# Optimization experiments

Hardware: AMD Instinct MI355X
Metric: run time of the kernel (lower is better)

## Reference

```python
import jax, jax.numpy as jnp
import numpy as np

B, S, D = 8, 2048, 512


def setup_inputs() -> dict:
    key = jax.random.key(0)
    ks = jax.random.split(key, 8)
    batch = jax.random.normal(ks[0], (B, S, D), dtype=jnp.float32)
    lengths = jax.random.randint(ks[1], (B,), 1, S + 1)  # in [1, S], avoid empty rows
    scale = 1.0 / np.sqrt(D)
    wq = jax.random.normal(ks[2], (D, D), dtype=jnp.float32) * scale
    bq = jnp.zeros((D,), dtype=jnp.float32)
    wk = jax.random.normal(ks[3], (D, D), dtype=jnp.float32) * scale
    bk = jnp.zeros((D,), dtype=jnp.float32)
    wv = jax.random.normal(ks[4], (D, D), dtype=jnp.float32) * scale
    bv = jnp.zeros((D,), dtype=jnp.float32)
    return {"batch": batch, "wq": wq, "bq": bq, "wk": wk, "bk": bk,
            "wv": wv, "bv": bv, "lengths": lengths}


def reference(batch, wq, bq, wk, bk, wv, bv, lengths):
    # Linear projections (torch nn.Linear: x @ W.T + b)
    q = batch @ wq.T + bq  # [B,S,D]
    k = batch @ wk.T + bk
    v = batch @ wv.T + bv
    d = batch.shape[-1]
    scores = jnp.einsum('bqd,bkd->bqk', q, k) / jnp.sqrt(jnp.asarray(d, batch.dtype))
    col = jnp.arange(scores.shape[-1])
    row = jnp.arange(scores.shape[-2])
    causal = col[None, :] <= row[:, None]                  # [S,S], allow col <= row
    pad = col[None, None, :] < lengths[:, None, None]      # [B,1,S], allow col < length
    mask = causal[None, :, :] & pad
    scores = jnp.where(mask, scores, -jnp.inf)
    attn = jax.nn.softmax(scores, axis=-1)
    return jnp.einsum('bqk,bkd->bqd', attn, v)
```

## Files before the change

kernel.cpp:

```cpp
#include <hip/hip_runtime.h>


typedef unsigned short u16;
typedef unsigned int u32;
typedef u16 u16x4 __attribute__((ext_vector_type(4)));
typedef float f32x4 __attribute__((ext_vector_type(4)));
typedef __bf16 bf16x8 __attribute__((ext_vector_type(8)));

#define NBATCH 8
#define NS 2048
#define ND 512
#define NM (NBATCH*NS)

typedef __attribute__((address_space(1))) u32 gu32;
typedef __attribute__((address_space(3))) u32 lu32;
#define GLD16(g, l) __builtin_amdgcn_global_load_lds((gu32*)(g), (lu32*)(l), 16, 0, 0)

__device__ __forceinline__ u16 f2bf(float f) {
  union { float f; u32 u; } v; v.f = f;
  u32 r = v.u + 0x7FFFu + ((v.u >> 16) & 1u);
  return (u16)(r >> 16);
}

__device__ __forceinline__ f32x4 mfma16(bf16x8 a, bf16x8 b, f32x4 c) {
  return __builtin_amdgcn_mfma_f32_16x16x32_bf16(a, b, c, 0, 0, 0);
}

__global__ void cvt_kernel(const float* __restrict__ batch,
                           const float* __restrict__ wq,
                           const float* __restrict__ wk,
                           const float* __restrict__ wv,
                           u16* __restrict__ Xb, u16* __restrict__ Wqb,
                           u16* __restrict__ Wkb, u16* __restrict__ Wvb) {
  const int MD4 = NM * ND / 4;
  const int W4 = ND * ND / 4;
  int total = MD4 + 3 * W4;
  for (int i = blockIdx.x * blockDim.x + threadIdx.x; i < total;
       i += gridDim.x * blockDim.x) {
    const float4* src; u16x4* dst; int off;
    if (i < MD4)             { src = (const float4*)batch; dst = (u16x4*)Xb;  off = i; }
    else if (i < MD4 + W4)   { src = (const float4*)wq;    dst = (u16x4*)Wqb; off = i - MD4; }
    else if (i < MD4 + 2*W4) { src = (const float4*)wk;    dst = (u16x4*)Wkb; off = i - MD4 - W4; }
    else                     { src = (const float4*)wv;    dst = (u16x4*)Wvb; off = i - MD4 - 2*W4; }
    float4 v = src[off];
    u16x4 o; o[0] = f2bf(v.x); o[1] = f2bf(v.y); o[2] = f2bf(v.z); o[3] = f2bf(v.w);
    dst[off] = o;
  }
}

__global__ __launch_bounds__(256) void qkv_gemm(
    const u16* __restrict__ Xb,
    const u16* __restrict__ Wqb, const u16* __restrict__ Wkb, const u16* __restrict__ Wvb,
    const float* __restrict__ bq, const float* __restrict__ bk, const float* __restrict__ bv,
    u16* __restrict__ Qb, u16* __restrict__ Kb, u16* __restrict__ Vt) {
  __shared__ u16 Asm[128 * 64];
  __shared__ u16 Bsm[128 * 64];
  int tid = threadIdx.x;
  int w = tid >> 6, lane = tid & 63, la = lane & 15, hi = lane >> 4;
  int wm = w >> 1, wn = w & 1;
  int m0 = blockIdx.x * 128, n0 = blockIdx.y * 128, z = blockIdx.z;
  const u16* W = (z == 0) ? Wqb : (z == 1) ? Wkb : Wvb;
  f32x4 acc[4][4];
  f32x4 zero = {0.f, 0.f, 0.f, 0.f};
#pragma unroll
  for (int mi = 0; mi < 4; ++mi)
#pragma unroll
    for (int ni = 0; ni < 4; ++ni) acc[mi][ni] = zero;

  for (int kt = 0; kt < 8; ++kt) {
#pragma unroll
    for (int i = 0; i < 4; ++i) {
      int c = w * 4 + i;
      int row = c * 8 + (lane >> 3);
      const char* ga = (const char*)Xb + ((size_t)(m0 + row) * ND + kt * 64) * 2 + (lane & 7) * 16;
      GLD16(ga, (char*)Asm + c * 1024);
      const char* gb = (const char*)W + ((size_t)(n0 + row) * ND + kt * 64) * 2 + (lane & 7) * 16;
      GLD16(gb, (char*)Bsm + c * 1024);
    }
    __syncthreads();
#pragma unroll
    for (int kk = 0; kk < 2; ++kk) {
      bf16x8 a[4], bfr[4];
#pragma unroll
      for (int mi = 0; mi < 4; ++mi)
        a[mi] = *(const bf16x8*)((const char*)Asm + (wm * 64 + mi * 16 + la) * 128 + kk * 64 + hi * 16);
#pragma unroll
      for (int ni = 0; ni < 4; ++ni)
        bfr[ni] = *(const bf16x8*)((const char*)Bsm + (wn * 64 + ni * 16 + la) * 128 + kk * 64 + hi * 16);
#pragma unroll
      for (int mi = 0; mi < 4; ++mi)
#pragma unroll
        for (int ni = 0; ni < 4; ++ni)
          acc[mi][ni] = mfma16(a[mi], bfr[ni], acc[mi][ni]);
    }
    __syncthreads();
  }

  const float* bias = (z == 0) ? bq : (z == 1) ? bk : bv;
  float scl = (z == 0) ? 0.044194173824159216f : 1.0f;
#pragma unroll
  for (int mi = 0; mi < 4; ++mi) {
#pragma unroll
    for (int ni = 0; ni < 4; ++ni) {
      int col = n0 + wn * 64 + ni * 16 + la;
      int rbase = m0 + wm * 64 + mi * 16 + hi * 4;
      float bc = bias[col];
      if (z == 2) {
        int bbx = rbase >> 11, s0 = rbase & 2047;
        u16x4 pk;
#pragma unroll
        for (int j = 0; j < 4; ++j) pk[j] = f2bf(acc[mi][ni][j] + bc);
        *(u16x4*)((char*)Vt + (((size_t)bbx * ND + col) * NS + s0) * 2) = pk;
      } else {
        u16* Ob = (z == 0) ? Qb : Kb;
#pragma unroll
        for (int j = 0; j < 4; ++j)
          Ob[(size_t)(rbase + j) * ND + col] = f2bf((acc[mi][ni][j] + bc) * scl);
      }
    }
  }
}

__global__ __launch_bounds__(256, 1) void attn_kernel(
    const u16* __restrict__ Qb, const u16* __restrict__ Kb, const u16* __restrict__ Vt,
    const int* __restrict__ lens, float* __restrict__ out) {
  __shared__ u16 Ksm[64 * 512];
  __shared__ u16 Vsm[512 * 64];
  __shared__ u16 Psm[4][16 * 72];
  int tid = threadIdx.x;
  int w = tid >> 6, lane = tid & 63, la = lane & 15, hi = lane >> 4;
  int b = blockIdx.y, q0 = blockIdx.x * 64;
  int len = lens[b];
  int r0 = q0 + w * 16;
  int qrow = r0 + la;

  bf16x8 qf[16];
  const char* qbase = (const char*)Qb + (size_t)(b * NS + r0 + la) * ND * 2 + hi * 16;
#pragma unroll
  for (int kc = 0; kc < 16; ++kc) qf[kc] = *(const bf16x8*)(qbase + kc * 64);

  f32x4 o[32];
  f32x4 zero = {0.f, 0.f, 0.f, 0.f};
#pragma unroll
  for (int i = 0; i < 32; ++i) o[i] = zero;
  float mrow = -1e30f, lrow = 0.f;

  int kmaxc = min(q0 + 63, len - 1);
  int ntiles = (kmaxc >> 6) + 1;

  for (int t = 0; t < ntiles; ++t) {
    int k0 = t * 64;
#pragma unroll
    for (int i = 0; i < 16; ++i) {
      int r = w * 16 + i;
      const char* g = (const char*)Kb + (size_t)(b * NS + k0 + r) * ND * 2 + ((lane ^ (r & 7)) * 16);
      GLD16(g, (char*)Ksm + r * 1024);
    }
#pragma unroll
    for (int i = 0; i < 16; ++i) {
      int c = w * 16 + i;
      int d = c * 8 + (lane >> 3);
      const char* g = (const char*)Vt + ((size_t)(b * ND + d) * NS + k0) * 2 + (((lane & 7) ^ (d & 7)) * 16);
      GLD16(g, (char*)Vsm + c * 1024);
    }
    __syncthreads();

    f32x4 s[4];
#pragma unroll
    for (int f = 0; f < 4; ++f) s[f] = zero;
#pragma unroll
    for (int kc = 0; kc < 16; ++kc) {
#pragma unroll
      for (int f = 0; f < 4; ++f) {
        int row = f * 16 + la;
        const char* p = (const char*)Ksm + row * 1024 + ((kc * 64 + hi * 16) ^ ((row & 7) * 16));
        bf16x8 kf = *(const bf16x8*)p;
        s[f] = mfma16(kf, qf[kc], s[f]);
      }
    }

    float tmax = -1e30f;
#pragma unroll
    for (int f = 0; f < 4; ++f) {
#pragma unroll
      for (int j = 0; j < 4; ++j) {
        int kabs = k0 + f * 16 + hi * 4 + j;
        bool ok = (kabs <= qrow) && (kabs < len);
        float vv = ok ? s[f][j] : -1e30f;
        s[f][j] = vv;
        tmax = fmaxf(tmax, vv);
      }
    }
    tmax = fmaxf(tmax, __shfl_xor(tmax, 16));
    tmax = fmaxf(tmax, __shfl_xor(tmax, 32));
    float mnew = fmaxf(mrow, tmax);
    float alpha = __expf(mrow - mnew);
    float psum = 0.f;
#pragma unroll
    for (int f = 0; f < 4; ++f) {
#pragma unroll
      for (int j = 0; j < 4; ++j) {
        float p = __expf(s[f][j] - mnew);
        s[f][j] = p;
        psum += p;
      }
    }
    psum += __shfl_xor(psum, 16);
    psum += __shfl_xor(psum, 32);
    lrow = lrow * alpha + psum;
    mrow = mnew;

#pragma unroll
    for (int f = 0; f < 4; ++f) {
      u16x4 pk;
#pragma unroll
      for (int j = 0; j < 4; ++j) pk[j] = f2bf(s[f][j]);
      *(u16x4*)((char*)&Psm[w][0] + la * 144 + (f * 16 + hi * 4) * 2) = pk;
    }

    float aj[4];
#pragma unroll
    for (int j = 0; j < 4; ++j) aj[j] = __shfl(alpha, hi * 4 + j);
#pragma unroll
    for (int nb = 0; nb < 32; ++nb) {
      o[nb][0] *= aj[0]; o[nb][1] *= aj[1]; o[nb][2] *= aj[2]; o[nb][3] *= aj[3];
    }

#pragma unroll
    for (int ks = 0; ks < 2; ++ks) {
      bf16x8 pf = *(const bf16x8*)((const char*)&Psm[w][0] + la * 144 + ks * 64 + hi * 16);
#pragma unroll
      for (int nb = 0; nb < 32; ++nb) {
        int d = nb * 16 + la;
        const char* vp = (const char*)Vsm + d * 128 + ((ks * 64 + hi * 16) ^ ((d & 7) * 16));
        bf16x8 vf = *(const bf16x8*)vp;
        o[nb] = mfma16(pf, vf, o[nb]);
      }
    }
    __syncthreads();
  }

  float linv[4];
#pragma unroll
  for (int j = 0; j < 4; ++j) linv[j] = 1.0f / __shfl(lrow, hi * 4 + j);
  float* ob = out + (size_t)(b * NS + r0 + hi * 4) * ND + la;
#pragma unroll
  for (int nb = 0; nb < 32; ++nb)
#pragma unroll
    for (int j = 0; j < 4; ++j)
      ob[(size_t)j * ND + nb * 16] = o[nb][j] * linv[j];
}

extern "C" void kernel_launch(void* const* d_in, const int* in_sizes, int n_in,
                              void* d_out, int out_size, void* d_ws, size_t ws_size,
                              hipStream_t stream) {
  const float* batch = (const float*)d_in[0];
  const float* wq = (const float*)d_in[1];
  const float* bq = (const float*)d_in[2];
  const float* wk = (const float*)d_in[3];
  const float* bk = (const float*)d_in[4];
  const float* wv = (const float*)d_in[5];
  const float* bv = (const float*)d_in[6];
  const int* lens = (const int*)d_in[7];

  char* ws = (char*)d_ws;
  u16* Xb  = (u16*)(ws + 0);
  u16* Wqb = (u16*)(ws + 16777216);
  u16* Wkb = (u16*)(ws + 17301504);
  u16* Wvb = (u16*)(ws + 17825792);
  u16* Qb  = (u16*)(ws + 18350080);
  u16* Kb  = (u16*)(ws + 35127296);
  u16* Vt  = (u16*)(ws + 51904512);

  cvt_kernel<<<dim3(2048), dim3(256), 0, stream>>>(batch, wq, wk, wv, Xb, Wqb, Wkb, Wvb);
  qkv_gemm<<<dim3(128, 4, 3), dim3(256), 0, stream>>>(Xb, Wqb, Wkb, Wvb, bq, bk, bv, Qb, Kb, Vt);
  attn_kernel<<<dim3(32, 8), dim3(256), 0, stream>>>(Qb, Kb, Vt, lens, (float*)d_out);
}
```

Baseline: 193.4 us.

## Split long causal KV ranges across two blocks, prefetch tiles, and combine partials

```diff
diff --git a/kernel.cpp b/kernel.cpp
--- a/kernel.cpp
+++ b/kernel.cpp
@@ -123,14 +123,34 @@
 
 __global__ __launch_bounds__(256, 1) void attn_kernel(
     const u16* __restrict__ Qb, const u16* __restrict__ Kb, const u16* __restrict__ Vt,
-    const int* __restrict__ lens, float* __restrict__ out) {
+    const int* __restrict__ lens, float* __restrict__ out,
+    float* __restrict__ pO, float* __restrict__ pM, float* __restrict__ pL) {
   __shared__ u16 Ksm[64 * 512];
   __shared__ u16 Vsm[512 * 64];
-  __shared__ u16 Psm[4][16 * 72];
+  __shared__ u16 Psm[64 * 72];
+  __shared__ float Alds[64];
+  __shared__ float Llds[64];
+
+  int bi = blockIdx.x;
+  int qt = 31 - (bi >> 4);
+  int jj0 = bi & 15;
+  int b = jj0 & 7, c = jj0 >> 3;
+  int len = lens[b];
+  int q0 = qt * 64;
+  int kmax = min(q0 + 63, len - 1);
+  int lastT = kmax >> 6;
+  int t0 = c * 16;
+  int t1 = min(lastT + 1, t0 + 16);
+  bool split = (qt >= 16);
+  int slot = split ? ((b * 16 + (qt - 16)) * 2 + c) : 0;
   int tid = threadIdx.x;
   int w = tid >> 6, lane = tid & 63, la = lane & 15, hi = lane >> 4;
-  int b = blockIdx.y, q0 = blockIdx.x * 64;
-  int len = lens[b];
+
+  if (t0 >= t1) {
+    if (split && tid < 64) { pM[slot * 64 + tid] = -1e30f; pL[slot * 64 + tid] = 0.f; }
+    return;
+  }
+
   int r0 = q0 + w * 16;
   int qrow = r0 + la;
 
@@ -139,31 +159,40 @@
 #pragma unroll
   for (int kc = 0; kc < 16; ++kc) qf[kc] = *(const bf16x8*)(qbase + kc * 64);
 
-  f32x4 o[32];
+  f32x4 o[4][8];
   f32x4 zero = {0.f, 0.f, 0.f, 0.f};
 #pragma unroll
-  for (int i = 0; i < 32; ++i) o[i] = zero;
+  for (int qb = 0; qb < 4; ++qb)
+#pragma unroll
+    for (int nb = 0; nb < 8; ++nb) o[qb][nb] = zero;
   float mrow = -1e30f, lrow = 0.f;
 
-  int kmaxc = min(q0 + 63, len - 1);
-  int ntiles = (kmaxc >> 6) + 1;
-
-  for (int t = 0; t < ntiles; ++t) {
+#define STAGE_K(T) {                                                            \
+  _Pragma("unroll")                                                             \
+  for (int i_ = 0; i_ < 16; ++i_) {                                             \
+    int r_ = w * 16 + i_;                                                       \
+    const char* g_ = (const char*)Kb + (size_t)(b * NS + (T) * 64 + r_) * ND * 2 \
+                     + ((lane ^ (r_ & 7)) * 16);                                \
+    GLD16(g_, (char*)Ksm + r_ * 1024);                                          \
+  } }
+#define STAGE_V(T) {                                                            \
+  _Pragma("unroll")                                                             \
+  for (int i_ = 0; i_ < 16; ++i_) {                                             \
+    int c_ = w * 16 + i_;                                                       \
+    int d_ = c_ * 8 + (lane >> 3);                                              \
+    const char* g_ = (const char*)Vt + ((size_t)(b * ND + d_) * NS + (T) * 64) * 2 \
+                     + (((lane & 7) ^ (d_ & 7)) * 16);                          \
+    GLD16(g_, (char*)Vsm + c_ * 1024);                                          \
+  } }
+
+  STAGE_K(t0);
+  STAGE_V(t0);
+
+  for (int t = t0; t < t1; ++t) {
     int k0 = t * 64;
-#pragma unroll
-    for (int i = 0; i < 16; ++i) {
-      int r = w * 16 + i;
-      const char* g = (const char*)Kb + (size_t)(b * NS + k0 + r) * ND * 2 + ((lane ^ (r & 7)) * 16);
-      GLD16(g, (char*)Ksm + r * 1024);
-    }
-#pragma unroll
-    for (int i = 0; i < 16; ++i) {
-      int c = w * 16 + i;
-      int d = c * 8 + (lane >> 3);
-      const char* g = (const char*)Vt + ((size_t)(b * ND + d) * NS + k0) * 2 + (((lane & 7) ^ (d & 7)) * 16);
-      GLD16(g, (char*)Vsm + c * 1024);
-    }
-    __syncthreads();
+    bool more = (t + 1 < t1);
+    asm volatile("s_waitcnt vmcnt(16)" ::: "memory");
+    __builtin_amdgcn_s_barrier();
 
     f32x4 s[4];
 #pragma unroll
@@ -178,6 +207,8 @@
         s[f] = mfma16(kf, qf[kc], s[f]);
       }
     }
+    __builtin_amdgcn_s_barrier();
+    if (more) STAGE_K(t + 1);
 
     float tmax = -1e30f;
 #pragma unroll
@@ -193,7 +224,7 @@
     }
     tmax = fmaxf(tmax, __shfl_xor(tmax, 16));
     tmax = fmaxf(tmax, __shfl_xor(tmax, 32));
-    float mnew = fmaxf(mrow, tmax);
+    float mnew = fmaxf(fmaxf(mrow, tmax), -1e20f);
     float alpha = __expf(mrow - mnew);
     float psum = 0.f;
 #pragma unroll
@@ -215,40 +246,111 @@
       u16x4 pk;
 #pragma unroll
       for (int j = 0; j < 4; ++j) pk[j] = f2bf(s[f][j]);
-      *(u16x4*)((char*)&Psm[w][0] + la * 144 + (f * 16 + hi * 4) * 2) = pk;
-    }
-
-    float aj[4];
-#pragma unroll
-    for (int j = 0; j < 4; ++j) aj[j] = __shfl(alpha, hi * 4 + j);
-#pragma unroll
-    for (int nb = 0; nb < 32; ++nb) {
-      o[nb][0] *= aj[0]; o[nb][1] *= aj[1]; o[nb][2] *= aj[2]; o[nb][3] *= aj[3];
-    }
+      *(u16x4*)((char*)Psm + (w * 16 + la) * 144 + (f * 16 + hi * 4) * 2) = pk;
+    }
+    if (hi == 0) Alds[w * 16 + la] = alpha;
+    asm volatile("s_waitcnt lgkmcnt(0)" ::: "memory");
+    if (more) { asm volatile("s_waitcnt vmcnt(16)" ::: "memory"); }
+    else      { asm volatile("s_waitcnt vmcnt(0)" ::: "memory"); }
+    __builtin_amdgcn_s_barrier();
+
+    float aq[4][4];
+#pragma unroll
+    for (int qb = 0; qb < 4; ++qb)
+#pragma unroll
+      for (int j = 0; j < 4; ++j) aq[qb][j] = Alds[qb * 16 + hi * 4 + j];
+#pragma unroll
+    for (int qb = 0; qb < 4; ++qb)
+#pragma unroll
+      for (int nb = 0; nb < 8; ++nb) {
+        o[qb][nb][0] *= aq[qb][0]; o[qb][nb][1] *= aq[qb][1];
+        o[qb][nb][2] *= aq[qb][2]; o[qb][nb][3] *= aq[qb][3];
+      }
 
 #pragma unroll
     for (int ks = 0; ks < 2; ++ks) {
-      bf16x8 pf = *(const bf16x8*)((const char*)&Psm[w][0] + la * 144 + ks * 64 + hi * 16);
-#pragma unroll
-      for (int nb = 0; nb < 32; ++nb) {
-        int d = nb * 16 + la;
-        const char* vp = (const char*)Vsm + d * 128 + ((ks * 64 + hi * 16) ^ ((d & 7) * 16));
-        bf16x8 vf = *(const bf16x8*)vp;
-        o[nb] = mfma16(pf, vf, o[nb]);
-      }
-    }
-    __syncthreads();
-  }
-
-  float linv[4];
-#pragma unroll
-  for (int j = 0; j < 4; ++j) linv[j] = 1.0f / __shfl(lrow, hi * 4 + j);
-  float* ob = out + (size_t)(b * NS + r0 + hi * 4) * ND + la;
-#pragma unroll
-  for (int nb = 0; nb < 32; ++nb)
-#pragma unroll
-    for (int j = 0; j < 4; ++j)
-      ob[(size_t)j * ND + nb * 16] = o[nb][j] * linv[j];
+      bf16x8 vf[8];
+#pragma unroll
+      for (int nb = 0; nb < 8; ++nb) {
+        int d = w * 128 + nb * 16 + la;
+        vf[nb] = *(const bf16x8*)((const char*)Vsm + d * 128 + ((ks * 64 + hi * 16) ^ ((d & 7) * 16)));
+      }
+#pragma unroll
+      for (int qb = 0; qb < 4; ++qb) {
+        bf16x8 pf = *(const bf16x8*)((const char*)Psm + (qb * 16 + la) * 144 + ks * 64 + hi * 16);
+#pragma unroll
+        for (int nb = 0; nb < 8; ++nb) o[qb][nb] = mfma16(pf, vf[nb], o[qb][nb]);
+      }
+    }
+    __builtin_amdgcn_s_barrier();
+    if (more) STAGE_V(t + 1);
+  }
+
+  if (split) {
+    if (hi == 0) { pM[slot * 64 + w * 16 + la] = mrow; pL[slot * 64 + w * 16 + la] = lrow; }
+    float* dst = pO + (size_t)slot * 32768;
+#pragma unroll
+    for (int qb = 0; qb < 4; ++qb)
+#pragma unroll
+      for (int nb = 0; nb < 8; ++nb) {
+        int d = w * 128 + nb * 16 + la;
+#pragma unroll
+        for (int j = 0; j < 4; ++j)
+          dst[(size_t)(qb * 16 + hi * 4 + j) * ND + d] = o[qb][nb][j];
+      }
+  } else {
+    if (hi == 0) Llds[w * 16 + la] = lrow;
+    asm volatile("s_waitcnt lgkmcnt(0)" ::: "memory");
+    __builtin_amdgcn_s_barrier();
+    float li[4][4];
+#pragma unroll
+    for (int qb = 0; qb < 4; ++qb)
+#pragma unroll
+      for (int j = 0; j < 4; ++j) li[qb][j] = 1.0f / Llds[qb * 16 + hi * 4 + j];
+    float* dst = out + ((size_t)b * NS + q0) * ND;
+#pragma unroll
+    for (int qb = 0; qb < 4; ++qb)
+#pragma unroll
+      for (int nb = 0; nb < 8; ++nb) {
+        int d = w * 128 + nb * 16 + la;
+#pragma unroll
+        for (int j = 0; j < 4; ++j)
+          dst[(size_t)(qb * 16 + hi * 4 + j) * ND + d] = o[qb][nb][j] * li[qb][j];
+      }
+  }
+#undef STAGE_K
+#undef STAGE_V
+}
+
+__global__ __launch_bounds__(256) void combine_kernel(
+    const float* __restrict__ pO, const float* __restrict__ pM,
+    const float* __restrict__ pL, float* __restrict__ out) {
+  int qt = 16 + blockIdx.x, b = blockIdx.y;
+  int s0 = (b * 16 + (qt - 16)) * 2;
+  int tid = threadIdx.x;
+  int row = tid >> 2, dp = tid & 3;
+  float m0 = pM[s0 * 64 + row], m1 = pM[(s0 + 1) * 64 + row];
+  float l0 = pL[s0 * 64 + row], l1 = pL[(s0 + 1) * 64 + row];
+  float m = fmaxf(m0, m1);
+  float a0 = __expf(m0 - m), a1 = __expf(m1 - m);
+  float linv = 1.0f / (l0 * a0 + l1 * a1);
+  const float4* O0 = (const float4*)(pO + (size_t)s0 * 32768) + row * 128 + dp * 32;
+  const float4* O1 = (const float4*)(pO + (size_t)(s0 + 1) * 32768) + row * 128 + dp * 32;
+  float4* Op = (float4*)(out + ((size_t)b * NS + qt * 64 + row) * ND) + dp * 32;
+  bool has1 = (l1 > 0.f);
+  float c0 = a0 * linv, c1 = a1 * linv;
+#pragma unroll 8
+  for (int k = 0; k < 32; ++k) {
+    float4 v = O0[k], r;
+    if (has1) {
+      float4 v1 = O1[k];
+      r.x = v.x * c0 + v1.x * c1; r.y = v.y * c0 + v1.y * c1;
+      r.z = v.z * c0 + v1.z * c1; r.w = v.w * c0 + v1.w * c1;
+    } else {
+      r.x = v.x * c0; r.y = v.y * c0; r.z = v.z * c0; r.w = v.w * c0;
+    }
+    Op[k] = r;
+  }
 }
 
 extern "C" void kernel_launch(void* const* d_in, const int* in_sizes, int n_in,
@@ -271,8 +373,12 @@
   u16* Qb  = (u16*)(ws + 18350080);
   u16* Kb  = (u16*)(ws + 35127296);
   u16* Vt  = (u16*)(ws + 51904512);
+  float* pO = (float*)(ws + 68681728);
+  float* pM = (float*)(ws + 102236160);
+  float* pL = (float*)(ws + 102301696);
 
   cvt_kernel<<<dim3(2048), dim3(256), 0, stream>>>(batch, wq, wk, wv, Xb, Wqb, Wkb, Wvb);
   qkv_gemm<<<dim3(128, 4, 3), dim3(256), 0, stream>>>(Xb, Wqb, Wkb, Wvb, bq, bk, bv, Qb, Kb, Vt);
-  attn_kernel<<<dim3(32, 8), dim3(256), 0, stream>>>(Qb, Kb, Vt, lens, (float*)d_out);
-}
+  attn_kernel<<<dim3(512), dim3(256), 0, stream>>>(Qb, Kb, Vt, lens, (float*)d_out, pO, pM, pL);
+  combine_kernel<<<dim3(16, 8), dim3(256), 0, stream>>>(pO, pM, pL, (float*)d_out);
+}
```

Result: slower. 254.5 us (+31.6%).

## Split attention KV range across two blocks and merge with combine kernel

Applied to the files above, without the earlier changes.

```diff
diff --git a/kernel.cpp b/kernel.cpp
--- a/kernel.cpp
+++ b/kernel.cpp
@@ -121,16 +121,37 @@
   }
 }
 
-__global__ __launch_bounds__(256, 1) void attn_kernel(
+__global__ __launch_bounds__(256, 2) void attn_kernel(
     const u16* __restrict__ Qb, const u16* __restrict__ Kb, const u16* __restrict__ Vt,
-    const int* __restrict__ lens, float* __restrict__ out) {
-  __shared__ u16 Ksm[64 * 512];
-  __shared__ u16 Vsm[512 * 64];
-  __shared__ u16 Psm[4][16 * 72];
+    const int* __restrict__ lens,
+    u16* __restrict__ pOh, float* __restrict__ pM, float* __restrict__ pL) {
+  __shared__ u16 Ksm[32 * 512];
+  __shared__ u16 Vsm[512 * 32];
+  __shared__ u16 Psm[64 * 40];
+  __shared__ float Alds[64];
+
+  int bi = blockIdx.x;
+  int b = bi & 7;
+  int h = bi >> 8;
+  int q8 = (bi >> 3) & 31;
+  int qt = h ? (31 - q8) : q8;
+  int c = h;
+  int len = lens[b];
+  int q0 = qt * 64;
+  int kmax = min(q0 + 63, len - 1);
+  int lastT = kmax >> 5;
+  int half = qt + 1;
+  int t0 = c * half;
+  int t1 = min(lastT + 1, t0 + half);
+  int slot = (b * 32 + qt) * 2 + c;
   int tid = threadIdx.x;
   int w = tid >> 6, lane = tid & 63, la = lane & 15, hi = lane >> 4;
-  int b = blockIdx.y, q0 = blockIdx.x * 64;
-  int len = lens[b];
+
+  if (t0 >= t1) {
+    if (tid < 64) { pM[slot * 64 + tid] = -1e30f; pL[slot * 64 + tid] = 0.f; }
+    return;
+  }
+
   int r0 = q0 + w * 16;
   int qrow = r0 + la;
 
@@ -139,39 +160,38 @@
 #pragma unroll
   for (int kc = 0; kc < 16; ++kc) qf[kc] = *(const bf16x8*)(qbase + kc * 64);
 
-  f32x4 o[32];
+  f32x4 o[4][8];
   f32x4 zero = {0.f, 0.f, 0.f, 0.f};
 #pragma unroll
-  for (int i = 0; i < 32; ++i) o[i] = zero;
+  for (int qb = 0; qb < 4; ++qb)
+#pragma unroll
+    for (int nb = 0; nb < 8; ++nb) o[qb][nb] = zero;
   float mrow = -1e30f, lrow = 0.f;
 
-  int kmaxc = min(q0 + 63, len - 1);
-  int ntiles = (kmaxc >> 6) + 1;
-
-  for (int t = 0; t < ntiles; ++t) {
-    int k0 = t * 64;
-#pragma unroll
-    for (int i = 0; i < 16; ++i) {
-      int r = w * 16 + i;
+  for (int t = t0; t < t1; ++t) {
+    int k0 = t * 32;
+#pragma unroll
+    for (int i = 0; i < 8; ++i) {
+      int r = w * 8 + i;
       const char* g = (const char*)Kb + (size_t)(b * NS + k0 + r) * ND * 2 + ((lane ^ (r & 7)) * 16);
       GLD16(g, (char*)Ksm + r * 1024);
     }
 #pragma unroll
-    for (int i = 0; i < 16; ++i) {
-      int c = w * 16 + i;
-      int d = c * 8 + (lane >> 3);
-      const char* g = (const char*)Vt + ((size_t)(b * ND + d) * NS + k0) * 2 + (((lane & 7) ^ (d & 7)) * 16);
-      GLD16(g, (char*)Vsm + c * 1024);
-    }
-    __syncthreads();
-
-    f32x4 s[4];
-#pragma unroll
-    for (int f = 0; f < 4; ++f) s[f] = zero;
+    for (int i = 0; i < 8; ++i) {
+      int c2 = w * 8 + i;
+      int d = c2 * 16 + (lane >> 2);
+      int kb = lane & 3;
+      const char* g = (const char*)Vt + ((size_t)(b * ND + d) * NS + k0 + ((kb ^ (d & 3)) * 8)) * 2;
+      GLD16(g, (char*)Vsm + c2 * 1024);
+    }
+    __syncthreads();
+
+    f32x4 s[2];
+    s[0] = zero; s[1] = zero;
 #pragma unroll
     for (int kc = 0; kc < 16; ++kc) {
 #pragma unroll
-      for (int f = 0; f < 4; ++f) {
+      for (int f = 0; f < 2; ++f) {
         int row = f * 16 + la;
         const char* p = (const char*)Ksm + row * 1024 + ((kc * 64 + hi * 16) ^ ((row & 7) * 16));
         bf16x8 kf = *(const bf16x8*)p;
@@ -181,7 +201,7 @@
 
     float tmax = -1e30f;
 #pragma unroll
-    for (int f = 0; f < 4; ++f) {
+    for (int f = 0; f < 2; ++f) {
 #pragma unroll
       for (int j = 0; j < 4; ++j) {
         int kabs = k0 + f * 16 + hi * 4 + j;
@@ -193,11 +213,11 @@
     }
     tmax = fmaxf(tmax, __shfl_xor(tmax, 16));
     tmax = fmaxf(tmax, __shfl_xor(tmax, 32));
-    float mnew = fmaxf(mrow, tmax);
+    float mnew = fmaxf(fmaxf(mrow, tmax), -1e20f);
     float alpha = __expf(mrow - mnew);
     float psum = 0.f;
 #pragma unroll
-    for (int f = 0; f < 4; ++f) {
+    for (int f = 0; f < 2; ++f) {
 #pragma unroll
       for (int j = 0; j < 4; ++j) {
         float p = __expf(s[f][j] - mnew);
@@ -211,44 +231,89 @@
     mrow = mnew;
 
 #pragma unroll
-    for (int f = 0; f < 4; ++f) {
+    for (int f = 0; f < 2; ++f) {
       u16x4 pk;
 #pragma unroll
       for (int j = 0; j < 4; ++j) pk[j] = f2bf(s[f][j]);
-      *(u16x4*)((char*)&Psm[w][0] + la * 144 + (f * 16 + hi * 4) * 2) = pk;
-    }
-
-    float aj[4];
-#pragma unroll
-    for (int j = 0; j < 4; ++j) aj[j] = __shfl(alpha, hi * 4 + j);
-#pragma unroll
-    for (int nb = 0; nb < 32; ++nb) {
-      o[nb][0] *= aj[0]; o[nb][1] *= aj[1]; o[nb][2] *= aj[2]; o[nb][3] *= aj[3];
-    }
-
-#pragma unroll
-    for (int ks = 0; ks < 2; ++ks) {
-      bf16x8 pf = *(const bf16x8*)((const char*)&Psm[w][0] + la * 144 + ks * 64 + hi * 16);
-#pragma unroll
-      for (int nb = 0; nb < 32; ++nb) {
-        int d = nb * 16 + la;
-        const char* vp = (const char*)Vsm + d * 128 + ((ks * 64 + hi * 16) ^ ((d & 7) * 16));
-        bf16x8 vf = *(const bf16x8*)vp;
-        o[nb] = mfma16(pf, vf, o[nb]);
-      }
-    }
-    __syncthreads();
-  }
-
-  float linv[4];
-#pragma unroll
-  for (int j = 0; j < 4; ++j) linv[j] = 1.0f / __shfl(lrow, hi * 4 + j);
-  float* ob = out + (size_t)(b * NS + r0 + hi * 4) * ND + la;
-#pragma unroll
-  for (int nb = 0; nb < 32; ++nb)
-#pragma unroll
-    for (int j = 0; j < 4; ++j)
-      ob[(size_t)j * ND + nb * 16] = o[nb][j] * linv[j];
+      *(u16x4*)((char*)Psm + (w * 16 + la) * 80 + f * 32 + hi * 8) = pk;
+    }
+    if (hi == 0) Alds[w * 16 + la] = alpha;
+    __syncthreads();
+
+    float aq[4][4];
+#pragma unroll
+    for (int qb = 0; qb < 4; ++qb)
+#pragma unroll
+      for (int j = 0; j < 4; ++j) aq[qb][j] = Alds[qb * 16 + hi * 4 + j];
+#pragma unroll
+    for (int qb = 0; qb < 4; ++qb)
+#pragma unroll
+      for (int nb = 0; nb < 8; ++nb) {
+        o[qb][nb][0] *= aq[qb][0]; o[qb][nb][1] *= aq[qb][1];
+        o[qb][nb][2] *= aq[qb][2]; o[qb][nb][3] *= aq[qb][3];
+      }
+
+    bf16x8 vf[8];
+#pragma unroll
+    for (int nb = 0; nb < 8; ++nb) {
+      int d = w * 128 + nb * 16 + la;
+      vf[nb] = *(const bf16x8*)((const char*)Vsm + d * 64 + ((hi ^ (d & 3)) * 16));
+    }
+#pragma unroll
+    for (int qb = 0; qb < 4; ++qb) {
+      bf16x8 pf = *(const bf16x8*)((const char*)Psm + (qb * 16 + la) * 80 + hi * 16);
+#pragma unroll
+      for (int nb = 0; nb < 8; ++nb) o[qb][nb] = mfma16(pf, vf[nb], o[qb][nb]);
+    }
+    __syncthreads();
+  }
+
+  if (hi == 0) { pM[slot * 64 + w * 16 + la] = mrow; pL[slot * 64 + w * 16 + la] = lrow; }
+  u16* dst = pOh + (size_t)slot * (64 * 512);
+#pragma unroll
+  for (int qb = 0; qb < 4; ++qb)
+#pragma unroll
+    for (int nb = 0; nb < 8; ++nb) {
+      int base = (qb * 16 + hi * 4) * 512 + w * 128 + nb * 16 + la;
+#pragma unroll
+      for (int j = 0; j < 4; ++j) dst[base + j * 512] = f2bf(o[qb][nb][j]);
+    }
+}
+
+__global__ __launch_bounds__(256) void combine_kernel(
+    const u16* __restrict__ pOh, const float* __restrict__ pM,
+    const float* __restrict__ pL, float* __restrict__ out) {
+  int qt = blockIdx.x, b = blockIdx.y;
+  int s0 = (b * 32 + qt) * 2;
+  int tid = threadIdx.x;
+  int row = tid >> 2, qq = tid & 3;
+  float m0 = pM[s0 * 64 + row], m1 = pM[(s0 + 1) * 64 + row];
+  float l0 = pL[s0 * 64 + row], l1 = pL[(s0 + 1) * 64 + row];
+  float m = fmaxf(m0, m1);
+  float a0 = __expf(m0 - m), a1 = __expf(m1 - m);
+  float linv = 1.0f / (l0 * a0 + l1 * a1);
+  float c0 = a0 * linv, c1 = a1 * linv;
+  bool has1 = (l1 > 0.f);
+  const uint4* O0 = (const uint4*)(pOh + (size_t)s0 * 32768) + row * 64 + qq * 16;
+  const uint4* O1 = (const uint4*)(pOh + (size_t)(s0 + 1) * 32768) + row * 64 + qq * 16;
+  float4* Op = (float4*)(out + ((size_t)b * NS + qt * 64 + row) * ND) + qq * 32;
+#pragma unroll 4
+  for (int k = 0; k < 16; ++k) {
+    uint4 v0 = O0[k];
+    uint4 v1 = has1 ? O1[k] : uint4{0, 0, 0, 0};
+    u32 w0[4] = {v0.x, v0.y, v0.z, v0.w};
+    u32 w1[4] = {v1.x, v1.y, v1.z, v1.w};
+    float4 r[2];
+#pragma unroll
+    for (int p = 0; p < 4; ++p) {
+      float f0lo = __uint_as_float(w0[p] << 16), f0hi = __uint_as_float(w0[p] & 0xFFFF0000u);
+      float f1lo = __uint_as_float(w1[p] << 16), f1hi = __uint_as_float(w1[p] & 0xFFFF0000u);
+      ((float*)r)[p * 2]     = f0lo * c0 + f1lo * c1;
+      ((float*)r)[p * 2 + 1] = f0hi * c0 + f1hi * c1;
+    }
+    Op[k * 2] = r[0];
+    Op[k * 2 + 1] = r[1];
+  }
 }
 
 extern "C" void kernel_launch(void* const* d_in, const int* in_sizes, int n_in,
@@ -264,15 +329,19 @@
   const int* lens = (const int*)d_in[7];
 
   char* ws = (char*)d_ws;
-  u16* Xb  = (u16*)(ws + 0);
-  u16* Wqb = (u16*)(ws + 16777216);
-  u16* Wkb = (u16*)(ws + 17301504);
-  u16* Wvb = (u16*)(ws + 17825792);
-  u16* Qb  = (u16*)(ws + 18350080);
-  u16* Kb  = (u16*)(ws + 35127296);
-  u16* Vt  = (u16*)(ws + 51904512);
+  u16* Qb  = (u16*)(ws + 0);
+  u16* Kb  = (u16*)(ws + 16777216);
+  u16* Vt  = (u16*)(ws + 33554432);
+  u16* Xb  = (u16*)(ws + 50331648);
+  u16* Wqb = (u16*)(ws + 67108864);
+  u16* Wkb = (u16*)(ws + 67633152);
+  u16* Wvb = (u16*)(ws + 68157440);
+  u16* pOh = (u16*)(ws + 50331648);
+  float* pM = (float*)(ws + 83886080);
+  float* pL = (float*)(ws + 84017152);
 
   cvt_kernel<<<dim3(2048), dim3(256), 0, stream>>>(batch, wq, wk, wv, Xb, Wqb, Wkb, Wvb);
   qkv_gemm<<<dim3(128, 4, 3), dim3(256), 0, stream>>>(Xb, Wqb, Wkb, Wvb, bq, bk, bv, Qb, Kb, Vt);
-  attn_kernel<<<dim3(32, 8), dim3(256), 0, stream>>>(Qb, Kb, Vt, lens, (float*)d_out);
-}
+  attn_kernel<<<dim3(512), dim3(256), 0, stream>>>(Qb, Kb, Vt, lens, pOh, pM, pL);
+  combine_kernel<<<dim3(32, 8), dim3(256), 0, stream>>>(pOh, pM, pL, (float*)d_out);
+}
```

Result: slower. 329.8 us (+70.5%).
